# Kernel tuning notes

Measured on AMD Instinct MI355X. Metric: run time of the kernel, lower is better.

Reference implementation:

```python
import jax, jax.numpy as jnp
from jax import lax
import numpy as np

N_CLUSTERS = 512
MAX_ITER = 10
N_SAMPLES = 400000
N_FEATURES = 128


def setup_inputs() -> dict:
    key = jax.random.key(0)
    kx, ki = jax.random.split(key)
    X = jax.random.normal(kx, (N_SAMPLES, N_FEATURES), dtype=jnp.float32)
    # init centroids = K random (with-replacement) rows of X, mimicking kmeans seeding
    idx = jax.random.randint(ki, (N_CLUSTERS,), 0, N_SAMPLES)
    init_centroids = X[idx]
    return {"X": X, "init_centroids": init_centroids}


def reference(X, init_centroids):
    """Lloyd's k-means: MAX_ITER iterations of cdist -> argmin -> segment-mean.
    Returns (cluster_centers [K,D], labels [N] int32, inertia scalar)."""
    K = init_centroids.shape[0]
    n = X.shape[0]
    x_sq = jnp.sum(X * X, axis=1, keepdims=True)            # [N,1], loop-invariant
    ones = jnp.ones((n,), dtype=X.dtype)

    def step(cent, _):
        c_sq = jnp.sum(cent * cent, axis=1)                  # [K]
        # squared euclidean distances (cdist^2); argmin/min order matches cdist
        d2 = x_sq - 2.0 * (X @ cent.T) + c_sq[None, :]       # [N,K]
        labels = jnp.argmin(d2, axis=1)                      # [N]
        inertia = jnp.sum(jnp.maximum(jnp.min(d2, axis=1), 0.0))
        sums = jax.ops.segment_sum(X, labels, num_segments=K)          # [K,D]
        counts = jax.ops.segment_sum(ones, labels, num_segments=K)     # [K]
        means = sums / jnp.maximum(counts, 1.0)[:, None]
        # empty cluster -> keep old centroid (torch branch: (labels==k).sum()>0)
        new_cent = jnp.where(counts[:, None] > 0, means, cent)
        return new_cent, (labels, inertia)

    centroids, (labels_hist, inertia_hist) = lax.scan(
        step, init_centroids, None, length=MAX_ITER)
    return centroids, labels_hist[-1], inertia_hist[-1]
```

## Files before the change

### kernel.cpp

```cpp
#include <hip/hip_runtime.h>

#define N_S 400000
#define N_F 128
#define N_K 512
#define ITERS 10

typedef __attribute__((ext_vector_type(8))) short short8;
typedef __attribute__((ext_vector_type(4))) float floatx4;

__device__ inline unsigned short f2bf(float f) {
    unsigned int u = __float_as_uint(f);
    unsigned int r = (u + 0x7FFFu + ((u >> 16) & 1u)) >> 16;
    return (unsigned short)r;
}

__device__ inline unsigned int cvt_pk_bf16(float lo, float hi) {
    unsigned int r;
    asm("v_cvt_pk_bf16_f32 %0, %1, %2" : "=v"(r) : "v"(lo), "v"(hi));
    return r;
}

__device__ inline void gload_lds16(const void* g, void* l) {
    __builtin_amdgcn_global_load_lds(
        (const __attribute__((address_space(1))) void*)g,
        (__attribute__((address_space(3))) void*)l, 16, 0, 0);
}

__device__ inline void put_sw(unsigned short* __restrict__ swhi, int k, int d, float v) {
    int c = k >> 5, mm = k & 31;
    int mt = mm >> 4, m = mm & 15;
    int kt = d >> 5, r = d & 31;
    int quad = r >> 3, j = r & 7;
    int lane = quad * 16 + m;
    int idx = ((c * 8 + mt * 4 + kt) * 64 + lane) * 8 + j;
    swhi[idx] = f2bf(v);
}

__global__ __launch_bounds__(64) void prep_update_kernel(
    const float* __restrict__ src, float* __restrict__ cent,
    float* __restrict__ sums, int* __restrict__ ihist,
    float* __restrict__ c_sq, unsigned short* __restrict__ swhi,
    int* __restrict__ cursor, float* __restrict__ inertia, int do_update) {
    int k = blockIdx.x, lane = threadIdx.x;
    float a, b;
    float cnt = (float)ihist[k];
    if (do_update) {
        float sa = sums[k * N_F + lane], sb = sums[k * N_F + 64 + lane];
        float olda = cent[k * N_F + lane], oldb = cent[k * N_F + 64 + lane];
        a = (cnt > 0.f) ? (sa / cnt) : olda;
        b = (cnt > 0.f) ? (sb / cnt) : oldb;
    } else {
        a = src[k * N_F + lane];
        b = src[k * N_F + 64 + lane];
    }
    cent[k * N_F + lane] = a;
    cent[k * N_F + 64 + lane] = b;
    sums[k * N_F + lane] = 0.f;
    sums[k * N_F + 64 + lane] = 0.f;
    put_sw(swhi, k, lane, a);
    put_sw(swhi, k, lane + 64, b);
    float s = fmaf(a, a, b * b);
#pragma unroll
    for (int off = 32; off > 0; off >>= 1) s += __shfl_down(s, off);
    if (lane == 0) {
        c_sq[k] = s;
        ihist[k] = 0;
        cursor[k] = 0;
        if (k == 0) *inertia = 0.f;
    }
}

#define CHUNK 32
#define NCHUNK (N_K / CHUNK)
#define NTN 4

__global__ __launch_bounds__(256, 2) void assign_kernel(
    const float* __restrict__ X,
    const unsigned short* __restrict__ swhi,
    const float* __restrict__ c_sq,
    float* __restrict__ labels,
    float* __restrict__ inertia,
    int* __restrict__ ihist) {
    __shared__ __align__(16) short8 a_lds[2][4 * 8 * 64];
    __shared__ __align__(16) float csq_s[N_K];
    __shared__ int lhist[N_K];
    __shared__ float red[4];

    int t = threadIdx.x;
    int w = t >> 6, l = t & 63;
    int quad = l >> 4, l15 = l & 15;
    long long S0 = (long long)blockIdx.x * 256;

    {
        const char* gq = (const char*)swhi + t * 16;
        char* lq = (char*)a_lds[0] + t * 16;
#pragma unroll
        for (int i = 0; i < 8; ++i) gload_lds16(gq + i * 4096, lq + i * 4096);
    }

    for (int i = t; i < N_K; i += 256) {
        lhist[i] = 0;
        csq_s[i] = c_sq[i];
    }

    short8 bhi[NTN][4];
    float xsqv[NTN];
    long long srow[NTN];
#pragma unroll
    for (int nt = 0; nt < NTN; ++nt) {
        long long s = S0 + w * 64 + nt * 16 + l15;
        srow[nt] = s;
        long long ss = (s < N_S) ? s : (N_S - 1);
        const float4* xp = (const float4*)(X + ss * N_F);
        float sq = 0.f;
#pragma unroll
        for (int kt = 0; kt < 4; ++kt) {
            float4 va = xp[kt * 8 + quad * 2];
            float4 vb = xp[kt * 8 + quad * 2 + 1];
            float f[8] = {va.x, va.y, va.z, va.w, vb.x, vb.y, vb.z, vb.w};
            short8 h;
            unsigned int* hw = (unsigned int*)&h;
            hw[0] = cvt_pk_bf16(f[0], f[1]);
            hw[1] = cvt_pk_bf16(f[2], f[3]);
            hw[2] = cvt_pk_bf16(f[4], f[5]);
            hw[3] = cvt_pk_bf16(f[6], f[7]);
#pragma unroll
            for (int j = 0; j < 8; ++j) sq = fmaf(f[j], f[j], sq);
            bhi[nt][kt] = h;
        }
        sq += __shfl_xor(sq, 16);
        sq += __shfl_xor(sq, 32);
        xsqv[nt] = sq;
    }

    __syncthreads();

    float best[NTN];
    int bestk[NTN];
#pragma unroll
    for (int nt = 0; nt < NTN; ++nt) { best[nt] = 3.4e38f; bestk[nt] = 0; }

#pragma unroll
    for (int p = 0; p < 4; ++p) {
        if (p < 3) {
            const char* gq = (const char*)swhi + (p + 1) * 32768 + t * 16;
            char* lq = (char*)a_lds[(p + 1) & 1] + t * 16;
#pragma unroll
            for (int i = 0; i < 8; ++i) gload_lds16(gq + i * 4096, lq + i * 4096);
        }

        const short8* abase = a_lds[p & 1] + l;
#pragma unroll
        for (int cc = 0; cc < 4; ++cc) {
            int c = p * 4 + cc;
            floatx4 acc[2][NTN];
#pragma unroll
            for (int mt = 0; mt < 2; ++mt)
#pragma unroll
                for (int nt = 0; nt < NTN; ++nt) acc[mt][nt] = (floatx4){0.f, 0.f, 0.f, 0.f};

#pragma unroll
            for (int kt = 0; kt < 4; ++kt) {
                short8 a0 = abase[(cc * 8 + kt) * 64];
                short8 a1 = abase[(cc * 8 + 4 + kt) * 64];
#pragma unroll
                for (int nt = 0; nt < NTN; ++nt) {
                    acc[0][nt] = __builtin_amdgcn_mfma_f32_16x16x32_bf16(a0, bhi[nt][kt], acc[0][nt], 0, 0, 0);
                    acc[1][nt] = __builtin_amdgcn_mfma_f32_16x16x32_bf16(a1, bhi[nt][kt], acc[1][nt], 0, 0, 0);
                }
            }

#pragma unroll
            for (int mt = 0; mt < 2; ++mt) {
                float4 cs = ((const float4*)csq_s)[c * 8 + mt * 4 + quad];
#pragma unroll
                for (int r = 0; r < 4; ++r) {
                    float csr = (r == 0) ? cs.x : (r == 1) ? cs.y : (r == 2) ? cs.z : cs.w;
                    int kg = c * CHUNK + mt * 16 + quad * 4 + r;
#pragma unroll
                    for (int nt = 0; nt < NTN; ++nt) {
                        float d2 = fmaf(-2.f, acc[mt][nt][r], csr);
                        if (d2 < best[nt]) { best[nt] = d2; bestk[nt] = kg; }
                    }
                }
            }
        }

        if (p < 3) __syncthreads();
    }

#pragma unroll
    for (int nt = 0; nt < NTN; ++nt) {
#pragma unroll
        for (int off = 16; off < 64; off <<= 1) {
            float ob = __shfl_xor(best[nt], off);
            int ok = __shfl_xor(bestk[nt], off);
            if (ob < best[nt] || (ob == best[nt] && ok < bestk[nt])) {
                best[nt] = ob;
                bestk[nt] = ok;
            }
        }
    }

    float contrib = 0.f;
    if (quad == 0) {
#pragma unroll
        for (int nt = 0; nt < NTN; ++nt) {
            if (srow[nt] < N_S) {
                labels[srow[nt]] = (float)bestk[nt];
                atomicAdd(&lhist[bestk[nt]], 1);
                contrib += fmaxf(xsqv[nt] + best[nt], 0.f);
            }
        }
    }
#pragma unroll
    for (int off = 32; off > 0; off >>= 1) contrib += __shfl_down(contrib, off);
    if (l == 0) red[w] = contrib;
    __syncthreads();
    if (t == 0) atomicAdd(inertia, red[0] + red[1] + red[2] + red[3]);

    for (int i = t; i < N_K; i += 256) {
        int v = lhist[i];
        if (v) atomicAdd(&ihist[i], v);
    }
}

__global__ __launch_bounds__(256) void scatter_kernel(const float* __restrict__ labels,
                                                      const int* __restrict__ ihist,
                                                      int* __restrict__ cursor,
                                                      int* __restrict__ order) {
    __shared__ int lhist[N_K];
    __shared__ int excl[N_K];
    __shared__ int lbase[N_K];
    __shared__ int wtot[4];
    int t = threadIdx.x;
    long long i0 = (long long)blockIdx.x * 1024 + (long long)t * 4;

    for (int j = t; j < N_K; j += 256) lhist[j] = 0;

    int v0 = ihist[2 * t], v1 = ihist[2 * t + 1];
    int s = v0 + v1;
    int x = s;
    int lane = t & 63, w = t >> 6;
#pragma unroll
    for (int off = 1; off < 64; off <<= 1) {
        int y = __shfl_up(x, off);
        if (lane >= off) x += y;
    }
    if (lane == 63) wtot[w] = x;
    __syncthreads();
    int woff = 0;
    for (int ww = 0; ww < w; ++ww) woff += wtot[ww];
    int ex = woff + x - s;
    excl[2 * t] = ex;
    excl[2 * t + 1] = ex + v0;

    int k0 = 0, k1 = 0, k2 = 0, k3 = 0, r0 = 0, r1 = 0, r2 = 0, r3 = 0;
    bool valid = (i0 < N_S);
    if (valid) {
        float4 lab = *(const float4*)(labels + i0);
        k0 = (int)lab.x; k1 = (int)lab.y; k2 = (int)lab.z; k3 = (int)lab.w;
        r0 = atomicAdd(&lhist[k0], 1);
        r1 = atomicAdd(&lhist[k1], 1);
        r2 = atomicAdd(&lhist[k2], 1);
        r3 = atomicAdd(&lhist[k3], 1);
    }
    __syncthreads();
    for (int j = t; j < N_K; j += 256) {
        int c = lhist[j];
        lbase[j] = c ? (excl[j] + atomicAdd(&cursor[j], c)) : 0;
    }
    __syncthreads();
    if (valid) {
        order[lbase[k0] + r0] = (int)i0;
        order[lbase[k1] + r1] = (int)i0 + 1;
        order[lbase[k2] + r2] = (int)i0 + 2;
        order[lbase[k3] + r3] = (int)i0 + 3;
    }
}

#define RPB 256
#define RPG 32

__device__ inline void flush4(float* __restrict__ sums, int k, int dbase, float4 acc) {
    float* sp = sums + k * N_F + dbase;
    atomicAdd(sp + 0, acc.x);
    atomicAdd(sp + 1, acc.y);
    atomicAdd(sp + 2, acc.z);
    atomicAdd(sp + 3, acc.w);
}

__global__ __launch_bounds__(256) void csum_kernel(const float* __restrict__ X,
                                                   const int* __restrict__ order,
                                                   const float* __restrict__ labels,
                                                   float* __restrict__ sums) {
    __shared__ int ord_s[RPB];
    __shared__ int k_s[RPB];
    int t = threadIdx.x;
    long long r0 = (long long)blockIdx.x * RPB;
    bool vrow = (r0 + t) < N_S;
    int o = vrow ? order[r0 + t] : 0;
    ord_s[t] = o;
    k_s[t] = vrow ? (int)labels[o] : N_K;
    __syncthreads();

    int g = t >> 5;
    int dbase = (t & 31) << 2;
    const float* Xd = X + dbase;
    int base = g * RPG;

    float4 acc = {0.f, 0.f, 0.f, 0.f};
    int kcur = k_s[base];
    if (kcur == k_s[base + RPG - 1]) {
#pragma unroll 8
        for (int i = 0; i < RPG; ++i) {
            const float4 v = *(const float4*)(Xd + (long long)ord_s[base + i] * N_F);
            acc.x += v.x; acc.y += v.y; acc.z += v.z; acc.w += v.w;
        }
        flush4(sums, kcur, dbase, acc);
    } else {
        for (int i = 0; i < RPG; ++i) {
            int k = k_s[base + i];
            if (k != kcur) {
                flush4(sums, kcur, dbase, acc);
                acc = (float4){0.f, 0.f, 0.f, 0.f};
                kcur = k;
            }
            const float4 v = *(const float4*)(Xd + (long long)ord_s[base + i] * N_F);
            acc.x += v.x; acc.y += v.y; acc.z += v.z; acc.w += v.w;
        }
        flush4(sums, kcur, dbase, acc);
    }
}

__global__ __launch_bounds__(128) void update_kernel(const float* __restrict__ sums,
                                                     const int* __restrict__ ihist,
                                                     float* __restrict__ cent) {
    int k = blockIdx.x;
    int d = threadIdx.x;
    float c = (float)ihist[k];
    float s = sums[k * N_F + d];
    float old = cent[k * N_F + d];
    cent[k * N_F + d] = (c > 0.f) ? (s / c) : old;
}

extern "C" void kernel_launch(void* const* d_in, const int* in_sizes, int n_in,
                              void* d_out, int out_size, void* d_ws, size_t ws_size,
                              hipStream_t stream) {
    const float* X = (const float*)d_in[0];
    const float* initc = (const float*)d_in[1];

    float* out = (float*)d_out;
    float* cent = out;
    float* labels = out + N_K * N_F;
    float* inertia = labels + N_S;

    float* c_sq = (float*)d_ws;
    float* sums = c_sq + N_K;
    unsigned short* swhi = (unsigned short*)(sums + (N_K + 1) * N_F);
    int* ihist = (int*)(swhi + N_K * N_F);
    int* cursor = ihist + N_K;
    int* order = cursor + N_K;

    for (int it = 0; it < ITERS; ++it) {
        prep_update_kernel<<<N_K, 64, 0, stream>>>(initc, cent, sums, ihist, c_sq,
                                                   swhi, cursor, inertia, it > 0);
        assign_kernel<<<(N_S + 255) / 256, 256, 0, stream>>>(X, swhi, c_sq,
                                                             labels, inertia, ihist);
        scatter_kernel<<<(N_S + 1023) / 1024, 256, 0, stream>>>(labels, ihist, cursor, order);
        csum_kernel<<<(N_S + RPB - 1) / RPB, 256, 0, stream>>>(X, order, labels, sums);
    }
    update_kernel<<<N_K, N_F, 0, stream>>>(sums, ihist, cent);
}
```

Baseline: 1.810 ms.

## Halve assign LDS stages for higher occupancy and pack labels into order entries

The assign kernel now stages centroid tiles in half-size LDS buffers over twice as many pipeline phases and raises the launch-bounds occupancy hint from 2 to 4 blocks. This cuts LDS use per block so more blocks can share a CU, at the cost of more barriers and more register pressure. The scatter kernel packs each row's cluster id into the low 9 bits of its order entry, so the cluster-sum kernel no longer does a dependent gather of labels. The cluster-sum kernel also uses smaller row groups, which means more blocks and more atomic flushes.

```diff
diff --git a/kernel.cpp b/kernel.cpp
--- a/kernel.cpp
+++ b/kernel.cpp
@@ -71,17 +71,16 @@
 }
 
 #define CHUNK 32
-#define NCHUNK (N_K / CHUNK)
 #define NTN 4
 
-__global__ __launch_bounds__(256, 2) void assign_kernel(
+__global__ __launch_bounds__(256, 4) void assign_kernel(
     const float* __restrict__ X,
     const unsigned short* __restrict__ swhi,
     const float* __restrict__ c_sq,
     float* __restrict__ labels,
     float* __restrict__ inertia,
     int* __restrict__ ihist) {
-    __shared__ __align__(16) short8 a_lds[2][4 * 8 * 64];
+    __shared__ __align__(16) short8 a_lds[2][2 * 8 * 64];
     __shared__ __align__(16) float csq_s[N_K];
     __shared__ int lhist[N_K];
     __shared__ float red[4];
@@ -95,7 +94,7 @@
         const char* gq = (const char*)swhi + t * 16;
         char* lq = (char*)a_lds[0] + t * 16;
 #pragma unroll
-        for (int i = 0; i < 8; ++i) gload_lds16(gq + i * 4096, lq + i * 4096);
+        for (int i = 0; i < 4; ++i) gload_lds16(gq + i * 4096, lq + i * 4096);
     }
 
     for (int i = t; i < N_K; i += 256) {
@@ -141,18 +140,18 @@
     for (int nt = 0; nt < NTN; ++nt) { best[nt] = 3.4e38f; bestk[nt] = 0; }
 
 #pragma unroll
-    for (int p = 0; p < 4; ++p) {
-        if (p < 3) {
-            const char* gq = (const char*)swhi + (p + 1) * 32768 + t * 16;
+    for (int p = 0; p < 8; ++p) {
+        if (p < 7) {
+            const char* gq = (const char*)swhi + (p + 1) * 16384 + t * 16;
             char* lq = (char*)a_lds[(p + 1) & 1] + t * 16;
 #pragma unroll
-            for (int i = 0; i < 8; ++i) gload_lds16(gq + i * 4096, lq + i * 4096);
+            for (int i = 0; i < 4; ++i) gload_lds16(gq + i * 4096, lq + i * 4096);
         }
 
         const short8* abase = a_lds[p & 1] + l;
 #pragma unroll
-        for (int cc = 0; cc < 4; ++cc) {
-            int c = p * 4 + cc;
+        for (int cc = 0; cc < 2; ++cc) {
+            int c = p * 2 + cc;
             floatx4 acc[2][NTN];
 #pragma unroll
             for (int mt = 0; mt < 2; ++mt)
@@ -186,7 +185,7 @@
             }
         }
 
-        if (p < 3) __syncthreads();
+        if (p < 7) __syncthreads();
     }
 
 #pragma unroll
@@ -272,15 +271,16 @@
     }
     __syncthreads();
     if (valid) {
-        order[lbase[k0] + r0] = (int)i0;
-        order[lbase[k1] + r1] = (int)i0 + 1;
-        order[lbase[k2] + r2] = (int)i0 + 2;
-        order[lbase[k3] + r3] = (int)i0 + 3;
-    }
-}
-
-#define RPB 256
-#define RPG 32
+        int i = (int)i0;
+        order[lbase[k0] + r0] = ((i + 0) << 9) | k0;
+        order[lbase[k1] + r1] = ((i + 1) << 9) | k1;
+        order[lbase[k2] + r2] = ((i + 2) << 9) | k2;
+        order[lbase[k3] + r3] = ((i + 3) << 9) | k3;
+    }
+}
+
+#define RPB 128
+#define RPG 16
 
 __device__ inline void flush4(float* __restrict__ sums, int k, int dbase, float4 acc) {
     float* sp = sums + k * N_F + dbase;
@@ -292,16 +292,11 @@
 
 __global__ __launch_bounds__(256) void csum_kernel(const float* __restrict__ X,
                                                    const int* __restrict__ order,
-                                                   const float* __restrict__ labels,
                                                    float* __restrict__ sums) {
     __shared__ int ord_s[RPB];
-    __shared__ int k_s[RPB];
     int t = threadIdx.x;
-    long long r0 = (long long)blockIdx.x * RPB;
-    bool vrow = (r0 + t) < N_S;
-    int o = vrow ? order[r0 + t] : 0;
-    ord_s[t] = o;
-    k_s[t] = vrow ? (int)labels[o] : N_K;
+    int r0 = blockIdx.x * RPB;
+    if (t < RPB) ord_s[t] = order[r0 + t];
     __syncthreads();
 
     int g = t >> 5;
@@ -310,23 +305,25 @@
     int base = g * RPG;
 
     float4 acc = {0.f, 0.f, 0.f, 0.f};
-    int kcur = k_s[base];
-    if (kcur == k_s[base + RPG - 1]) {
-#pragma unroll 8
+    int kcur = ord_s[base] & 511;
+    if (kcur == (ord_s[base + RPG - 1] & 511)) {
+#pragma unroll
         for (int i = 0; i < RPG; ++i) {
-            const float4 v = *(const float4*)(Xd + (long long)ord_s[base + i] * N_F);
+            int row = ord_s[base + i] >> 9;
+            const float4 v = *(const float4*)(Xd + (long long)row * N_F);
             acc.x += v.x; acc.y += v.y; acc.z += v.z; acc.w += v.w;
         }
         flush4(sums, kcur, dbase, acc);
     } else {
         for (int i = 0; i < RPG; ++i) {
-            int k = k_s[base + i];
+            int e = ord_s[base + i];
+            int k = e & 511;
             if (k != kcur) {
                 flush4(sums, kcur, dbase, acc);
                 acc = (float4){0.f, 0.f, 0.f, 0.f};
                 kcur = k;
             }
-            const float4 v = *(const float4*)(Xd + (long long)ord_s[base + i] * N_F);
+            const float4 v = *(const float4*)(Xd + (long long)(e >> 9) * N_F);
             acc.x += v.x; acc.y += v.y; acc.z += v.z; acc.w += v.w;
         }
         flush4(sums, kcur, dbase, acc);
@@ -368,7 +365,7 @@
         assign_kernel<<<(N_S + 255) / 256, 256, 0, stream>>>(X, swhi, c_sq,
                                                              labels, inertia, ihist);
         scatter_kernel<<<(N_S + 1023) / 1024, 256, 0, stream>>>(labels, ihist, cursor, order);
-        csum_kernel<<<(N_S + RPB - 1) / RPB, 256, 0, stream>>>(X, order, labels, sums);
+        csum_kernel<<<N_S / RPB, 256, 0, stream>>>(X, order, sums);
     }
     update_kernel<<<N_K, N_F, 0, stream>>>(sums, ihist, cent);
 }
```

New measurement: 2.674 ms. 1.48x slower.
